# Performance work log

Measured on AMD Instinct MI355X. Metric: run time of the kernel, lower is better.

Reference implementation:

```python
import jax, jax.numpy as jnp
import numpy as np

EMBED = 256
NUM_DEPTH = 128
NUM_CAMS = 1


def _bilinear_sample(img, x, y):
    # img: [H, W, E]; x, y: [L] pixel coords (align_corners=False, zero padding)
    H, W, _ = img.shape
    x0f = jnp.floor(x); y0f = jnp.floor(y)
    ix0 = x0f.astype(jnp.int32); iy0 = y0f.astype(jnp.int32)
    ix1 = ix0 + 1; iy1 = iy0 + 1
    wx1 = x - x0f; wx0 = 1.0 - wx1
    wy1 = y - y0f; wy0 = 1.0 - wy1

    def g(iy, ix):
        valid = (ix >= 0) & (ix < W) & (iy >= 0) & (iy < H)
        v = img[jnp.clip(iy, 0, H - 1), jnp.clip(ix, 0, W - 1)]  # [L, E]
        return jnp.where(valid[:, None], v, jnp.zeros((), img.dtype))

    return (g(iy0, ix0) * (wy0 * wx0)[:, None] + g(iy0, ix1) * (wy0 * wx1)[:, None]
            + g(iy1, ix0) * (wy1 * wx0)[:, None] + g(iy1, ix1) * (wy1 * wx1)[:, None])


def setup_inputs() -> dict:
    rng = jax.random.key(0)
    ks = jax.random.split(rng, 7)
    H = W = 64
    nv = H * W           # num_value == num_query (forced by output*key broadcast)
    bsv = 1
    return {
        "query": jax.random.normal(ks[0], (bsv, nv, EMBED), jnp.float32),
        "key": jax.random.normal(ks[1], (NUM_CAMS, nv, bsv, EMBED), jnp.float32),
        "value": jax.random.normal(ks[2], (NUM_CAMS, nv, bsv, EMBED), jnp.float32),
        "identity": jax.random.normal(ks[3], (bsv, nv, NUM_DEPTH), jnp.float32),
        "ref_3d": jax.random.uniform(ks[4], (bsv * NUM_CAMS, nv * NUM_DEPTH, 2), jnp.float32),
        "spatial_shapes": jnp.array([[H, W]], jnp.int32),
        "W_attn": jax.random.normal(ks[5], (NUM_CAMS * NUM_DEPTH, EMBED), jnp.float32) * 0.02,
        "b_attn": jax.random.normal(ks[6], (NUM_CAMS * NUM_DEPTH,), jnp.float32) * 0.02,
    }


def reference(query, key, value, identity, ref_3d, spatial_shapes, W_attn, b_attn):
    bsv, num_query, _ = query.shape
    num_cams, num_value, bs, _ = key.shape
    H = int(spatial_shapes[0, 0]); W = int(spatial_shapes[0, 1])

    # key/value rearrange (value flipped over cams dim, a no-op for num_cams=1)
    key_r = jnp.transpose(key, (2, 0, 1, 3)).reshape(bsv, num_value, EMBED)
    val_r = jnp.transpose(value[::-1], (2, 0, 1, 3)).reshape(bsv * num_cams, num_value, EMBED)

    # attention weights: Linear -> softmax over (levels*points)=1 axis (== ones)
    aw = query @ W_attn.T + b_attn                               # [bsv, nq, cams*depth]
    aw = aw.reshape(bsv, num_query, num_cams, NUM_DEPTH, 1, 1)    # heads=1, lv*pt=1
    aw = jax.nn.softmax(aw, axis=-1)
    aw = jnp.transpose(aw.reshape(bsv, num_query, num_cams, NUM_DEPTH, 1, 1, 1),
                       (0, 2, 1, 3, 4, 5, 6))
    aw = aw.reshape(bsv * num_cams, num_query * NUM_DEPTH)        # [B, L]

    # deformable bilinear sampling (single level/head/point)
    grids = 2.0 * ref_3d - 1.0                                   # grid_sample convention
    px = ((grids[..., 0] + 1.0) * W - 1.0) / 2.0                  # [B, L]
    py = ((grids[..., 1] + 1.0) * H - 1.0) / 2.0
    imgs = val_r.reshape(bsv * num_cams, H, W, EMBED)
    sampled = jax.vmap(_bilinear_sample)(imgs, px, py)            # [B, L, E]

    out = sampled * aw[:, :, None]                                # weighted gather
    out = out.reshape(bsv, num_cams, num_query, NUM_DEPTH, EMBED).mean(axis=1)

    # elementwise dot with key features, scaled
    out = jnp.sum(out * key_r[:, :, None, :], axis=-1) / jnp.sqrt(jnp.float32(EMBED))
    return out + identity                                         # [bsv, nq, num_depth]
```

## Files before the change

### kernel.cpp

```cpp
#include <hip/hip_runtime.h>

#define EMBED 256
#define NUM_DEPTH 128
#define CT_STRIDE 136

typedef __attribute__((ext_vector_type(8))) short bf16x8;
typedef __attribute__((ext_vector_type(4))) float f32x4;

__device__ __forceinline__ unsigned short f2b(float f) {
    union { float f; unsigned u; } c; c.f = f;
    unsigned u = c.u;
    u += 0x7fffu + ((u >> 16) & 1u);
    return (unsigned short)(u >> 16);
}
__device__ __forceinline__ float b2f(unsigned short h) {
    union { unsigned u; float f; } c; c.u = ((unsigned)h) << 16;
    return c.f;
}

__global__ __launch_bounds__(256) void cvt_kernel(
    const float4* __restrict__ key, const float4* __restrict__ val,
    ushort4* __restrict__ kb, ushort4* __restrict__ vb, int n4)
{
    int i = blockIdx.x * blockDim.x + threadIdx.x;
    if (i >= n4) return;
    float4 a = key[i];
    float4 b = val[i];
    kb[i] = make_ushort4(f2b(a.x), f2b(a.y), f2b(a.z), f2b(a.w));
    vb[i] = make_ushort4(f2b(b.x), f2b(b.y), f2b(b.z), f2b(b.w));
}

__global__ __launch_bounds__(256) void gemm_nt_bf16(
    const unsigned short* __restrict__ A,
    const unsigned short* __restrict__ B,
    unsigned short* __restrict__ D,
    int N)
{
    __shared__ __align__(16) unsigned short Ct[128 * CT_STRIDE];
    unsigned short* As = Ct;
    unsigned short* Bs = Ct + 8192;

    const int m0 = blockIdx.y * 128;
    const int n0 = blockIdx.x * 128;
    const int tid  = threadIdx.x;
    const int lane = tid & 63;
    const int wave = tid >> 6;
    const int wm = (wave & 1) * 64;
    const int wn = (wave >> 1) * 64;
    const int fm = lane & 15;
    const int kg = lane >> 4;

    f32x4 acc[4][4] = {};

    int srow[4], scol[4];
    #pragma unroll
    for (int j = 0; j < 4; ++j) {
        const int linear = j * 2048 + wave * 512 + lane * 8;
        srow[j] = linear >> 6;
        const int gl = (linear >> 3) & 7;
        scol[j] = ((gl ^ (srow[j] & 7)) << 3);
    }

    for (int kt = 0; kt < EMBED; kt += 64) {
        #pragma unroll
        for (int j = 0; j < 4; ++j) {
            __builtin_amdgcn_global_load_lds(
                (const __attribute__((address_space(1))) void*)
                    (A + (size_t)(m0 + srow[j]) * EMBED + kt + scol[j]),
                (__attribute__((address_space(3))) void*)(As + j * 2048 + wave * 512),
                16, 0, 0);
            __builtin_amdgcn_global_load_lds(
                (const __attribute__((address_space(1))) void*)
                    (B + (size_t)(n0 + srow[j]) * EMBED + kt + scol[j]),
                (__attribute__((address_space(3))) void*)(Bs + j * 2048 + wave * 512),
                16, 0, 0);
        }
        __syncthreads();

        #pragma unroll
        for (int s = 0; s < 2; ++s) {
            bf16x8 af[4], bfr[4];
            #pragma unroll
            for (int i = 0; i < 4; ++i) {
                const int ra = wm + i * 16 + fm;
                af[i]  = *(const bf16x8*)(As + ra * 64 + (((s * 4 + kg) ^ (ra & 7)) << 3));
                const int rb = wn + i * 16 + fm;
                bfr[i] = *(const bf16x8*)(Bs + rb * 64 + (((s * 4 + kg) ^ (rb & 7)) << 3));
            }
            #pragma unroll
            for (int i = 0; i < 4; ++i)
                #pragma unroll
                for (int j = 0; j < 4; ++j)
                    acc[i][j] = __builtin_amdgcn_mfma_f32_16x16x32_bf16(af[i], bfr[j], acc[i][j], 0, 0, 0);
        }
        __syncthreads();
    }

    const int col = lane & 15;
    const int rbase = kg * 4;
    #pragma unroll
    for (int i = 0; i < 4; ++i)
        #pragma unroll
        for (int j = 0; j < 4; ++j) {
            const int rr = wm + i * 16 + rbase;
            const int cc = wn + j * 16 + col;
            #pragma unroll
            for (int r = 0; r < 4; ++r)
                Ct[(rr + r) * CT_STRIDE + cc] = f2b(acc[i][j][r]);
        }
    __syncthreads();

    #pragma unroll
    for (int it = 0; it < 8; ++it) {
        const int r  = it * 16 + (tid >> 4);
        const int c8 = (tid & 15) * 8;
        const int4 v = *(const int4*)(Ct + r * CT_STRIDE + c8);
        *(int4*)(D + (size_t)(m0 + r) * N + n0 + c8) = v;
    }
}

__global__ __launch_bounds__(256) void gather_kernel(
    const unsigned short* __restrict__ D,
    const float* __restrict__ identity,
    const float* __restrict__ ref3d,
    const int*   __restrict__ spatial,
    float* __restrict__ out, int nv)
{
    __shared__ unsigned short Ds[2 * 4096];

    const int q0 = blockIdx.x * 2;
    const int tid = threadIdx.x;

    const int4* src = (const int4*)(D + (size_t)q0 * nv);
    int4* dst = (int4*)Ds;
    const int nchunk = (2 * nv) / 8;
    for (int i = tid; i < nchunk; i += 256) dst[i] = src[i];
    __syncthreads();

    const int Hs = spatial[0], Ws = spatial[1];
    const int l = q0 * NUM_DEPTH + tid;
    const int qi = tid >> 7;

    const float2 r2 = reinterpret_cast<const float2*>(ref3d)[l];
    const float px = r2.x * (float)Ws - 0.5f;
    const float py = r2.y * (float)Hs - 0.5f;
    const float x0f = floorf(px), y0f = floorf(py);
    const int ix0 = (int)x0f, iy0 = (int)y0f;
    const int ix1 = ix0 + 1,  iy1 = iy0 + 1;
    const float wx1 = px - x0f, wx0 = 1.0f - wx1;
    const float wy1 = py - y0f, wy0 = 1.0f - wy1;
    const bool vx0 = (ix0 >= 0) & (ix0 < Ws);
    const bool vx1 = (ix1 >= 0) & (ix1 < Ws);

    const unsigned short* row = Ds + qi * nv;
    float acc = 0.f;
    if (iy0 >= 0 && iy0 < Hs) {
        if (vx0) acc = fmaf(wy0 * wx0, b2f(row[iy0 * Ws + ix0]), acc);
        if (vx1) acc = fmaf(wy0 * wx1, b2f(row[iy0 * Ws + ix1]), acc);
    }
    if (iy1 >= 0 && iy1 < Hs) {
        if (vx0) acc = fmaf(wy1 * wx0, b2f(row[iy1 * Ws + ix0]), acc);
        if (vx1) acc = fmaf(wy1 * wx1, b2f(row[iy1 * Ws + ix1]), acc);
    }
    out[l] = fmaf(acc, 0.0625f, identity[l]);
}

__global__ __launch_bounds__(256) void uv_direct_kernel(
    const float* __restrict__ key, const float* __restrict__ value,
    const float* __restrict__ identity, const float* __restrict__ ref3d,
    const int* __restrict__ spatial, float* __restrict__ out)
{
    const int q = blockIdx.x;
    const int tid = threadIdx.x;
    const int lane = tid & 63;
    const int wave = tid >> 6;
    const int H = spatial[0], W = spatial[1];
    const int row4 = EMBED / 4;
    const float4 k4 = reinterpret_cast<const float4*>(key + (size_t)q * EMBED)[lane];
    const float4* __restrict__ v4 = reinterpret_cast<const float4*>(value);
    for (int d = wave; d < NUM_DEPTH; d += 4) {
        const int l = q * NUM_DEPTH + d;
        const float rx = ref3d[2 * l], ry = ref3d[2 * l + 1];
        const float px = rx * (float)W - 0.5f, py = ry * (float)H - 0.5f;
        const float x0f = floorf(px), y0f = floorf(py);
        const int ix0 = (int)x0f, iy0 = (int)y0f, ix1 = ix0 + 1, iy1 = iy0 + 1;
        const float wx1 = px - x0f, wx0 = 1.f - wx1, wy1 = py - y0f, wy0 = 1.f - wy1;
        float4 acc = make_float4(0.f, 0.f, 0.f, 0.f);
        #define TAP(IY, IX, WGT) \
            if ((IY) >= 0 && (IY) < H && (IX) >= 0 && (IX) < W) { \
                const float w_ = (WGT); \
                const float4 t = v4[(size_t)((IY) * W + (IX)) * row4 + lane]; \
                acc.x = fmaf(w_, t.x, acc.x); acc.y = fmaf(w_, t.y, acc.y); \
                acc.z = fmaf(w_, t.z, acc.z); acc.w = fmaf(w_, t.w, acc.w); }
        TAP(iy0, ix0, wy0 * wx0) TAP(iy0, ix1, wy0 * wx1)
        TAP(iy1, ix0, wy1 * wx0) TAP(iy1, ix1, wy1 * wx1)
        #undef TAP
        float partial = acc.x * k4.x + acc.y * k4.y + acc.z * k4.z + acc.w * k4.w;
        #pragma unroll
        for (int off = 32; off > 0; off >>= 1) partial += __shfl_xor(partial, off, 64);
        if (lane == 0) out[l] = fmaf(partial, 0.0625f, identity[l]);
    }
}

extern "C" void kernel_launch(void* const* d_in, const int* in_sizes, int n_in,
                              void* d_out, int out_size, void* d_ws, size_t ws_size,
                              hipStream_t stream) {
    const float* key      = (const float*)d_in[1];
    const float* value    = (const float*)d_in[2];
    const float* identity = (const float*)d_in[3];
    const float* ref3d    = (const float*)d_in[4];
    const int*   spatial  = (const int*)d_in[5];
    float* out = (float*)d_out;

    const int nq = in_sizes[3] / NUM_DEPTH;
    const int nv = in_sizes[1] / EMBED;

    const size_t d_bytes  = (size_t)nq * nv * sizeof(unsigned short);
    const size_t kb_bytes = (size_t)nq * EMBED * sizeof(unsigned short);
    const size_t vb_bytes = (size_t)nv * EMBED * sizeof(unsigned short);
    const size_t need = d_bytes + kb_bytes + vb_bytes;

    if (ws_size < need || (nq % 128) || (nv % 128) || nv > 4096 || (nq % 2) || nq != nv) {
        uv_direct_kernel<<<nq, 256, 0, stream>>>(key, value, identity, ref3d, spatial, out);
        return;
    }

    unsigned short* D  = (unsigned short*)d_ws;
    unsigned short* kb = (unsigned short*)((char*)d_ws + d_bytes);
    unsigned short* vb = (unsigned short*)((char*)d_ws + d_bytes + kb_bytes);

    const int n4 = nq * EMBED / 4;
    cvt_kernel<<<(n4 + 255) / 256, 256, 0, stream>>>(
        (const float4*)key, (const float4*)value, (ushort4*)kb, (ushort4*)vb, n4);

    dim3 grid(nv / 128, nq / 128);
    gemm_nt_bf16<<<grid, 256, 0, stream>>>(kb, vb, D, nv);

    gather_kernel<<<nq / 2, 256, 0, stream>>>(D, identity, ref3d, spatial, out, nv);
}
```

Baseline: 99.64 us.

## Fuse convert, GEMM and gather into one cooperative persistent kernel

```diff
diff --git a/kernel.cpp b/kernel.cpp
--- a/kernel.cpp
+++ b/kernel.cpp
@@ -1,4 +1,7 @@
 #include <hip/hip_runtime.h>
+#include <hip/hip_cooperative_groups.h>
+
+namespace cg = cooperative_groups;
 
 #define EMBED 256
 #define NUM_DEPTH 128
@@ -16,6 +19,164 @@
 __device__ __forceinline__ float b2f(unsigned short h) {
     union { unsigned u; float f; } c; c.u = ((unsigned)h) << 16;
     return c.f;
+}
+
+__global__ __launch_bounds__(256) void fused_kernel(
+    const float* __restrict__ key, const float* __restrict__ value,
+    const float* __restrict__ identity, const float* __restrict__ ref3d,
+    const int* __restrict__ spatial, float* __restrict__ out,
+    unsigned short* __restrict__ kb, unsigned short* __restrict__ vb,
+    unsigned short* __restrict__ D, int nq, int nv)
+{
+    __shared__ __align__(16) unsigned short Ct[128 * CT_STRIDE];
+    unsigned short* As = Ct;
+    unsigned short* Bs = Ct + 8192;
+
+    const int tid  = threadIdx.x;
+    const int bid  = blockIdx.x;
+    const int nblk = gridDim.x;
+    cg::grid_group grid = cg::this_grid();
+
+    {
+        const int n4 = nq * (EMBED / 4);
+        const float4* kf = (const float4*)key;
+        const float4* vf = (const float4*)value;
+        ushort4* ko = (ushort4*)kb;
+        ushort4* vo = (ushort4*)vb;
+        for (int i = bid * 256 + tid; i < n4; i += nblk * 256) {
+            float4 a = kf[i], b = vf[i];
+            ko[i] = make_ushort4(f2b(a.x), f2b(a.y), f2b(a.z), f2b(a.w));
+            vo[i] = make_ushort4(f2b(b.x), f2b(b.y), f2b(b.z), f2b(b.w));
+        }
+    }
+    grid.sync();
+
+    {
+        const int lane = tid & 63;
+        const int wave = tid >> 6;
+        const int NBx = nv >> 7;
+        const int ntile = (nq >> 7) * NBx;
+        const int wm = (wave & 1) * 64;
+        const int wn = (wave >> 1) * 64;
+        const int fm = lane & 15;
+        const int kg = lane >> 4;
+
+        int srow[4], scol[4];
+        #pragma unroll
+        for (int j = 0; j < 4; ++j) {
+            const int linear = j * 2048 + wave * 512 + lane * 8;
+            srow[j] = linear >> 6;
+            const int gl = (linear >> 3) & 7;
+            scol[j] = ((gl ^ (srow[j] & 7)) << 3);
+        }
+
+        for (int t = bid; t < ntile; t += nblk) {
+            const int m0 = (t / NBx) * 128;
+            const int n0 = (t % NBx) * 128;
+            f32x4 acc[4][4] = {};
+            __syncthreads();
+
+            for (int kt = 0; kt < EMBED; kt += 64) {
+                #pragma unroll
+                for (int j = 0; j < 4; ++j) {
+                    __builtin_amdgcn_global_load_lds(
+                        (const __attribute__((address_space(1))) void*)
+                            (kb + (size_t)(m0 + srow[j]) * EMBED + kt + scol[j]),
+                        (__attribute__((address_space(3))) void*)(As + j * 2048 + wave * 512),
+                        16, 0, 0);
+                    __builtin_amdgcn_global_load_lds(
+                        (const __attribute__((address_space(1))) void*)
+                            (vb + (size_t)(n0 + srow[j]) * EMBED + kt + scol[j]),
+                        (__attribute__((address_space(3))) void*)(Bs + j * 2048 + wave * 512),
+                        16, 0, 0);
+                }
+                __syncthreads();
+
+                #pragma unroll
+                for (int s = 0; s < 2; ++s) {
+                    bf16x8 af[4], bfr[4];
+                    #pragma unroll
+                    for (int i = 0; i < 4; ++i) {
+                        const int ra = wm + i * 16 + fm;
+                        af[i]  = *(const bf16x8*)(As + ra * 64 + (((s * 4 + kg) ^ (ra & 7)) << 3));
+                        const int rb = wn + i * 16 + fm;
+                        bfr[i] = *(const bf16x8*)(Bs + rb * 64 + (((s * 4 + kg) ^ (rb & 7)) << 3));
+                    }
+                    #pragma unroll
+                    for (int i = 0; i < 4; ++i)
+                        #pragma unroll
+                        for (int j = 0; j < 4; ++j)
+                            acc[i][j] = __builtin_amdgcn_mfma_f32_16x16x32_bf16(af[i], bfr[j], acc[i][j], 0, 0, 0);
+                }
+                __syncthreads();
+            }
+
+            const int col = lane & 15;
+            const int rbase = kg * 4;
+            #pragma unroll
+            for (int i = 0; i < 4; ++i)
+                #pragma unroll
+                for (int j = 0; j < 4; ++j) {
+                    const int rr = wm + i * 16 + rbase;
+                    const int cc = wn + j * 16 + col;
+                    #pragma unroll
+                    for (int r = 0; r < 4; ++r)
+                        Ct[(rr + r) * CT_STRIDE + cc] = f2b(acc[i][j][r]);
+                }
+            __syncthreads();
+
+            #pragma unroll
+            for (int it = 0; it < 8; ++it) {
+                const int r  = it * 16 + (tid >> 4);
+                const int c8 = (tid & 15) * 8;
+                const int4 v = *(const int4*)(Ct + r * CT_STRIDE + c8);
+                *(int4*)(D + (size_t)(m0 + r) * nv + n0 + c8) = v;
+            }
+        }
+    }
+    grid.sync();
+
+    {
+        const int Hs = spatial[0], Ws = spatial[1];
+        const int ngrp = nq >> 2;
+        for (int g = bid; g < ngrp; g += nblk) {
+            __syncthreads();
+            const int q0 = g * 4;
+            const int4* src = (const int4*)(D + (size_t)q0 * nv);
+            int4* dst = (int4*)Ct;
+            const int nchunk = (4 * nv) >> 3;
+            for (int i = tid; i < nchunk; i += 256) dst[i] = src[i];
+            __syncthreads();
+
+            #pragma unroll
+            for (int h = 0; h < 2; ++h) {
+                const int o = h * 256 + tid;
+                const int l = q0 * NUM_DEPTH + o;
+                const int qi = o >> 7;
+                const float2 r2 = reinterpret_cast<const float2*>(ref3d)[l];
+                const float px = r2.x * (float)Ws - 0.5f;
+                const float py = r2.y * (float)Hs - 0.5f;
+                const float x0f = floorf(px), y0f = floorf(py);
+                const int ix0 = (int)x0f, iy0 = (int)y0f;
+                const int ix1 = ix0 + 1,  iy1 = iy0 + 1;
+                const float wx1 = px - x0f, wx0 = 1.0f - wx1;
+                const float wy1 = py - y0f, wy0 = 1.0f - wy1;
+                const bool vx0 = (ix0 >= 0) & (ix0 < Ws);
+                const bool vx1 = (ix1 >= 0) & (ix1 < Ws);
+                const unsigned short* row = Ct + qi * nv;
+                float acc = 0.f;
+                if (iy0 >= 0 && iy0 < Hs) {
+                    if (vx0) acc = fmaf(wy0 * wx0, b2f(row[iy0 * Ws + ix0]), acc);
+                    if (vx1) acc = fmaf(wy0 * wx1, b2f(row[iy0 * Ws + ix1]), acc);
+                }
+                if (iy1 >= 0 && iy1 < Hs) {
+                    if (vx0) acc = fmaf(wy1 * wx0, b2f(row[iy1 * Ws + ix0]), acc);
+                    if (vx1) acc = fmaf(wy1 * wx1, b2f(row[iy1 * Ws + ix1]), acc);
+                }
+                out[l] = fmaf(acc, 0.0625f, identity[l]);
+            }
+        }
+    }
 }
 
 __global__ __launch_bounds__(256) void cvt_kernel(
@@ -33,8 +194,7 @@
 __global__ __launch_bounds__(256) void gemm_nt_bf16(
     const unsigned short* __restrict__ A,
     const unsigned short* __restrict__ B,
-    unsigned short* __restrict__ D,
-    int N)
+    unsigned short* __restrict__ D, int N)
 {
     __shared__ __align__(16) unsigned short Ct[128 * CT_STRIDE];
     unsigned short* As = Ct;
@@ -220,7 +380,7 @@
     const size_t vb_bytes = (size_t)nv * EMBED * sizeof(unsigned short);
     const size_t need = d_bytes + kb_bytes + vb_bytes;
 
-    if (ws_size < need || (nq % 128) || (nv % 128) || nv > 4096 || (nq % 2) || nq != nv) {
+    if (ws_size < need || (nq % 128) || (nv % 128) || nv > 4096 || (nq % 4) || nq != nv) {
         uv_direct_kernel<<<nq, 256, 0, stream>>>(key, value, identity, ref3d, spatial, out);
         return;
     }
@@ -229,12 +389,35 @@
     unsigned short* kb = (unsigned short*)((char*)d_ws + d_bytes);
     unsigned short* vb = (unsigned short*)((char*)d_ws + d_bytes + kb_bytes);
 
+    static int coopBlocks = -2;
+    if (coopBlocks == -2) {
+        int per = 0, dev = 0;
+        hipDeviceProp_t prop;
+        if (hipOccupancyMaxActiveBlocksPerMultiprocessor(&per, fused_kernel, 256, 0) == hipSuccess
+            && per > 0
+            && hipGetDevice(&dev) == hipSuccess
+            && hipGetDeviceProperties(&prop, dev) == hipSuccess)
+            coopBlocks = per * prop.multiProcessorCount;
+        else
+            coopBlocks = 0;
+    }
+
+    const int ntile = (nq / 128) * (nv / 128);
+    if (coopBlocks > 0) {
+        int nblk = coopBlocks < ntile ? coopBlocks : ntile;
+        void* args[] = { (void*)&key, (void*)&value, (void*)&identity, (void*)&ref3d,
+                         (void*)&spatial, (void*)&out, (void*)&kb, (void*)&vb,
+                         (void*)&D, (void*)&nq, (void*)&nv };
+        if (hipLaunchCooperativeKernel((void*)fused_kernel, dim3(nblk), dim3(256),
+                                       args, 0, stream) == hipSuccess)
+            return;
+        coopBlocks = 0;
+    }
+
     const int n4 = nq * EMBED / 4;
     cvt_kernel<<<(n4 + 255) / 256, 256, 0, stream>>>(
         (const float4*)key, (const float4*)value, (ushort4*)kb, (ushort4*)vb, n4);
-
     dim3 grid(nv / 128, nq / 128);
     gemm_nt_bf16<<<grid, 256, 0, stream>>>(kb, vb, D, nv);
-
     gather_kernel<<<nq / 2, 256, 0, stream>>>(D, identity, ref3d, spatial, out, nv);
 }
```

Measured after the change: 191.9 us. +92.6%, slower.

## Fuse bilinear gather into GEMM via per-row atomic completion counters

Applied to the files above, without the earlier changes.

```diff
diff --git a/kernel.cpp b/kernel.cpp
--- a/kernel.cpp
+++ b/kernel.cpp
@@ -6,6 +6,9 @@
 
 typedef __attribute__((ext_vector_type(8))) short bf16x8;
 typedef __attribute__((ext_vector_type(4))) float f32x4;
+
+__device__ int g_row_cnt[32];
+__device__ int g_row_done[32];
 
 __device__ __forceinline__ unsigned short f2b(float f) {
     union { float f; unsigned u; } c; c.f = f;
@@ -30,17 +33,24 @@
     vb[i] = make_ushort4(f2b(b.x), f2b(b.y), f2b(b.z), f2b(b.w));
 }
 
-__global__ __launch_bounds__(256) void gemm_nt_bf16(
+__global__ __launch_bounds__(256) void gemm_gather(
     const unsigned short* __restrict__ A,
     const unsigned short* __restrict__ B,
     unsigned short* __restrict__ D,
+    const float* __restrict__ identity,
+    const float* __restrict__ ref3d,
+    const int*   __restrict__ spatial,
+    float* __restrict__ out,
     int N)
 {
     __shared__ __align__(16) unsigned short Ct[128 * CT_STRIDE];
     unsigned short* As = Ct;
     unsigned short* Bs = Ct + 8192;
-
-    const int m0 = blockIdx.y * 128;
+    __shared__ int s_sig;
+
+    const int NBx = gridDim.x;
+    const int row = blockIdx.y;
+    const int m0 = row * 128;
     const int n0 = blockIdx.x * 128;
     const int tid  = threadIdx.x;
     const int lane = tid & 63;
@@ -117,52 +127,69 @@
         const int4 v = *(const int4*)(Ct + r * CT_STRIDE + c8);
         *(int4*)(D + (size_t)(m0 + r) * N + n0 + c8) = v;
     }
-}
-
-__global__ __launch_bounds__(256) void gather_kernel(
-    const unsigned short* __restrict__ D,
-    const float* __restrict__ identity,
-    const float* __restrict__ ref3d,
-    const int*   __restrict__ spatial,
-    float* __restrict__ out, int nv)
-{
-    __shared__ unsigned short Ds[2 * 4096];
-
-    const int q0 = blockIdx.x * 2;
-    const int tid = threadIdx.x;
-
-    const int4* src = (const int4*)(D + (size_t)q0 * nv);
-    int4* dst = (int4*)Ds;
-    const int nchunk = (2 * nv) / 8;
-    for (int i = tid; i < nchunk; i += 256) dst[i] = src[i];
+    __syncthreads();
+
+    if (tid == 0) {
+        __threadfence();
+        s_sig = atomicAdd(&g_row_cnt[row], 1);
+    }
+    __syncthreads();
+    const int old = s_sig;
+    if (old < NBx - 8) return;
+    const int slice = old - (NBx - 8);
+
+    if (tid == 0) {
+        while (__hip_atomic_load(&g_row_cnt[row], __ATOMIC_RELAXED,
+                                 __HIP_MEMORY_SCOPE_AGENT) < NBx)
+            __builtin_amdgcn_s_sleep(2);
+        __threadfence();
+    }
     __syncthreads();
 
     const int Hs = spatial[0], Ws = spatial[1];
-    const int l = q0 * NUM_DEPTH + tid;
     const int qi = tid >> 7;
-
-    const float2 r2 = reinterpret_cast<const float2*>(ref3d)[l];
-    const float px = r2.x * (float)Ws - 0.5f;
-    const float py = r2.y * (float)Hs - 0.5f;
-    const float x0f = floorf(px), y0f = floorf(py);
-    const int ix0 = (int)x0f, iy0 = (int)y0f;
-    const int ix1 = ix0 + 1,  iy1 = iy0 + 1;
-    const float wx1 = px - x0f, wx0 = 1.0f - wx1;
-    const float wy1 = py - y0f, wy0 = 1.0f - wy1;
-    const bool vx0 = (ix0 >= 0) & (ix0 < Ws);
-    const bool vx1 = (ix1 >= 0) & (ix1 < Ws);
-
-    const unsigned short* row = Ds + qi * nv;
-    float acc = 0.f;
-    if (iy0 >= 0 && iy0 < Hs) {
-        if (vx0) acc = fmaf(wy0 * wx0, b2f(row[iy0 * Ws + ix0]), acc);
-        if (vx1) acc = fmaf(wy0 * wx1, b2f(row[iy0 * Ws + ix1]), acc);
-    }
-    if (iy1 >= 0 && iy1 < Hs) {
-        if (vx0) acc = fmaf(wy1 * wx0, b2f(row[iy1 * Ws + ix0]), acc);
-        if (vx1) acc = fmaf(wy1 * wx1, b2f(row[iy1 * Ws + ix1]), acc);
-    }
-    out[l] = fmaf(acc, 0.0625f, identity[l]);
+    for (int g = 0; g < 8; ++g) {
+        const int q0 = m0 + slice * 16 + g * 2;
+        const int4* src = (const int4*)(D + (size_t)q0 * N);
+        int4* dst = (int4*)Ct;
+        const int nchunk = (2 * N) >> 3;
+        for (int i = tid; i < nchunk; i += 256) dst[i] = src[i];
+        __syncthreads();
+
+        const int l = q0 * NUM_DEPTH + tid;
+        const float2 r2 = reinterpret_cast<const float2*>(ref3d)[l];
+        const float px = r2.x * (float)Ws - 0.5f;
+        const float py = r2.y * (float)Hs - 0.5f;
+        const float x0f = floorf(px), y0f = floorf(py);
+        const int ix0 = (int)x0f, iy0 = (int)y0f;
+        const int ix1 = ix0 + 1,  iy1 = iy0 + 1;
+        const float wx1 = px - x0f, wx0 = 1.0f - wx1;
+        const float wy1 = py - y0f, wy0 = 1.0f - wy1;
+        const bool vx0 = (ix0 >= 0) & (ix0 < Ws);
+        const bool vx1 = (ix1 >= 0) & (ix1 < Ws);
+
+        const unsigned short* rowp = Ct + qi * N;
+        float accv = 0.f;
+        if (iy0 >= 0 && iy0 < Hs) {
+            if (vx0) accv = fmaf(wy0 * wx0, b2f(rowp[iy0 * Ws + ix0]), accv);
+            if (vx1) accv = fmaf(wy0 * wx1, b2f(rowp[iy0 * Ws + ix1]), accv);
+        }
+        if (iy1 >= 0 && iy1 < Hs) {
+            if (vx0) accv = fmaf(wy1 * wx0, b2f(rowp[iy1 * Ws + ix0]), accv);
+            if (vx1) accv = fmaf(wy1 * wx1, b2f(rowp[iy1 * Ws + ix1]), accv);
+        }
+        out[l] = fmaf(accv, 0.0625f, identity[l]);
+        __syncthreads();
+    }
+
+    if (tid == 0) {
+        if (atomicAdd(&g_row_done[row], 1) == 7) {
+            __hip_atomic_store(&g_row_cnt[row], 0, __ATOMIC_RELAXED,
+                               __HIP_MEMORY_SCOPE_AGENT);
+            __hip_atomic_store(&g_row_done[row], 0, __ATOMIC_RELAXED,
+                               __HIP_MEMORY_SCOPE_AGENT);
+        }
+    }
 }
 
 __global__ __launch_bounds__(256) void uv_direct_kernel(
@@ -220,7 +247,8 @@
     const size_t vb_bytes = (size_t)nv * EMBED * sizeof(unsigned short);
     const size_t need = d_bytes + kb_bytes + vb_bytes;
 
-    if (ws_size < need || (nq % 128) || (nv % 128) || nv > 4096 || (nq % 2) || nq != nv) {
+    if (ws_size < need || (nq % 128) || (nv % 128) || nv > 4096 || nq > 4096 ||
+        nq != nv || (nv / 128) < 9) {
         uv_direct_kernel<<<nq, 256, 0, stream>>>(key, value, identity, ref3d, spatial, out);
         return;
     }
@@ -234,7 +262,5 @@
         (const float4*)key, (const float4*)value, (ushort4*)kb, (ushort4*)vb, n4);
 
     dim3 grid(nv / 128, nq / 128);
-    gemm_nt_bf16<<<grid, 256, 0, stream>>>(kb, vb, D, nv);
-
-    gather_kernel<<<nq / 2, 256, 0, stream>>>(D, identity, ref3d, spatial, out, nv);
-}
+    gemm_gather<<<grid, 256, 0, stream>>>(kb, vb, D, identity, ref3d, spatial, out, nv);
+}
```

Measured after the change: 173.6 us. 1.74x slower.
